# Performance work log

Measured on AMD Instinct MI355X. Metric: run time of the kernel, lower is better.

## Reference

```python
import jax, jax.numpy as jnp
import numpy as np

N = 49104   # anchors (from hardcoded [2, 49104, 80] in source)
C = 80      # classes
K = 100     # max detections kept per class (fixed for jit-able output shapes)
SCORE_THRESH = 0.05
IOU_THRESH = 0.5


def setup_inputs() -> dict:
    key = jax.random.key(0)
    k1, k2 = jax.random.split(key)
    scores = jax.random.uniform(k1, (N, C), dtype=jnp.float32)
    # build valid xyxy boxes inside an ~800x800 image
    r = jax.random.uniform(k2, (N, 4), dtype=jnp.float32)
    x1 = r[:, 0] * 768.0
    y1 = r[:, 1] * 768.0
    w = r[:, 2] * 96.0 + 4.0
    h = r[:, 3] * 96.0 + 4.0
    boxes = jnp.stack([x1, y1, x1 + w, y1 + h], axis=1)
    return {"scores": scores, "boxes": boxes}


def _nms_all(scores, boxes):
    """Per-class greedy NMS, vectorized over classes via vmap.
    scores: [N, C], boxes: [N, 4] xyxy. Returns idxs/scs/valid each [C, K]."""
    areas = (boxes[:, 2] - boxes[:, 0]) * (boxes[:, 3] - boxes[:, 1])  # [N]

    def iou_vs_all(b, b_area):  # b: [4]
        ix1 = jnp.maximum(b[0], boxes[:, 0])
        iy1 = jnp.maximum(b[1], boxes[:, 1])
        ix2 = jnp.minimum(b[2], boxes[:, 2])
        iy2 = jnp.minimum(b[3], boxes[:, 3])
        inter = jnp.clip(ix2 - ix1, 0.0) * jnp.clip(iy2 - iy1, 0.0)
        return inter / (b_area + areas - inter + 1e-8)  # [N]

    def nms_one_class(s_c):  # s_c: [N]
        # score threshold (matches `scores > 0.05` masking in the torch loop)
        s0 = jnp.where(s_c > SCORE_THRESH, s_c, -jnp.inf)

        def step(s, _):
            idx = jnp.argmax(s)
            sc = s[idx]
            keep = jnp.isfinite(sc)  # anything left above threshold?
            ious = iou_vs_all(boxes[idx], areas[idx])
            suppress = (ious > IOU_THRESH) & keep
            s_next = jnp.where(suppress, -jnp.inf, s).at[idx].set(-jnp.inf)
            return s_next, (idx, sc, keep)

        _, (idxs, scs, keeps) = jax.lax.scan(step, s0, None, length=K)
        return idxs, scs, keeps  # each [K]

    return jax.vmap(nms_one_class)(scores.T)  # map over C classes


def reference(scores, boxes):
    idxs, scs, valids = _nms_all(scores, boxes)  # [C, K] each
    idxs = idxs.reshape(-1)                       # [C*K]
    valids = valids.reshape(-1)                   # [C*K] bool
    final_scores = jnp.where(valids, scs.reshape(-1), 0.0)        # [C*K]
    final_classes = jnp.repeat(jnp.arange(C, dtype=jnp.int32), K)  # [C*K]
    final_boxes = boxes[idxs] * valids[:, None].astype(boxes.dtype)  # [C*K, 4]
    return final_scores, final_classes, final_boxes, valids
```

## Files before the change

kernel.cpp:

```cpp
#include <hip/hip_runtime.h>
#include <math.h>
#include <stdint.h>

#define N_ANCH 49104
#define NCLS 80
#define KDET 100
#define CAP 256
#define TPB 512
#define NBINS 1024
#define NPROD 384
#define NBLK NPROD
#define NCONS NCLS
#define GRID (NPROD + NCONS)
#define SUBCAP 16
#define THETA 0.996090f
#define QTOT (N_ANCH * NCLS / 4)
#define JMAX 16
#define FLAG_MAGIC 0x5AC10000u
#define PADKEY(t) ((0xFFFFFFFFull << 16) | (uint64_t)(t))

#define LIST_ELEMS ((size_t)NCLS * NBLK * SUBCAP)
#define SUBCNT_OFF (LIST_ELEMS * 8)
#define FLAGS_OFF (SUBCNT_OFF + (size_t)NCLS * NBLK * 4)
#define WS_NEED (FLAGS_OFF + (size_t)NPROD * 4)

__device__ __forceinline__ void st_agent_u64(uint64_t* p, uint64_t v) {
    __hip_atomic_store(p, v, __ATOMIC_RELAXED, __HIP_MEMORY_SCOPE_AGENT);
}
__device__ __forceinline__ void st_agent_u32(int* p, int v) {
    __hip_atomic_store(p, v, __ATOMIC_RELAXED, __HIP_MEMORY_SCOPE_AGENT);
}
__device__ __forceinline__ uint64_t ld_agent_u64(const uint64_t* p) {
    return __hip_atomic_load(p, __ATOMIC_RELAXED, __HIP_MEMORY_SCOPE_AGENT);
}
__device__ __forceinline__ int ld_agent_i32(const int* p) {
    return __hip_atomic_load(p, __ATOMIC_RELAXED, __HIP_MEMORY_SCOPE_AGENT);
}
__device__ __forceinline__ uint32_t ld_agent_flag(const uint32_t* p) {
    return __hip_atomic_load(p, __ATOMIC_RELAXED, __HIP_MEMORY_SCOPE_AGENT);
}

__device__ __forceinline__ void collect_quad(int q, float4 v, int* lcnt,
                                             uint64_t* __restrict__ list, int blk) {
    const int n = q / 20;
    const int c0 = 4 * (q % 20);
    float ss[4] = {v.x, v.y, v.z, v.w};
#pragma unroll
    for (int u = 0; u < 4; u++) {
        float s = ss[u];
        if (s > THETA) {
            int c = c0 + u;
            int p = atomicAdd(&lcnt[c], 1);
            if (p < SUBCAP) {
                uint32_t bits = __float_as_uint(s);
                st_agent_u64(&list[((size_t)c * NBLK + blk) * SUBCAP + p],
                             ((uint64_t)(~bits) << 16) | (uint64_t)n);
            }
        }
    }
}

struct ChunkShared {
    uint64_t keys[CAP];
    float4   rbox[CAP];
    float    ra[CAP], rs[CAP];
    uint64_t smat[CAP * (CAP / 64)];
    uint64_t lwbuf[CAP / 64];
    uint64_t s_kw[CAP / 64];
    int      s_cw[4];
    float4   kbox[KDET];
    float    kar[KDET], ksc[KDET];
};

__device__ __forceinline__ int process_chunk(ChunkShared& S, int tid, int M, int kc0,
                                             const float* __restrict__ boxes) {
    if (M <= 0) return kc0;
    const int lane = tid & 63, wid = tid >> 6;
    if (tid < CAP) {
        const uint64_t key = S.keys[tid];
        const int n = (int)(key & 0xFFFFull);
        const int nc = n < N_ANCH ? n : N_ANCH - 1;
        const float4 mybox = *(const float4*)(boxes + (size_t)nc * 4);
        int rank = 0;
#pragma unroll 8
        for (int j = 0; j < CAP; j++) rank += (S.keys[j] < key) ? 1 : 0;
        S.rbox[rank] = mybox;
        S.ra[rank] = (mybox.z - mybox.x) * (mybox.w - mybox.y);
        S.rs[rank] = __uint_as_float(~((uint32_t)(key >> 16)));
    }
    __syncthreads();
    bool alive = (tid < M);
    if (alive && kc0 > 0) {
        float4 b = S.rbox[tid];
        float arb = S.ra[tid];
        for (int k2 = 0; k2 < kc0; k2++) {
            float4 kb = S.kbox[k2];
            float ix1 = fmaxf(kb.x, b.x), iy1 = fmaxf(kb.y, b.y);
            float ix2 = fminf(kb.z, b.z), iy2 = fminf(kb.w, b.w);
            float inter = fmaxf(ix2 - ix1, 0.0f) * fmaxf(iy2 - iy1, 0.0f);
            float iou = inter / (S.kar[k2] + arb - inter + 1e-8f);
            if (iou > 0.5f) { alive = false; break; }
        }
    }
    {
        uint64_t bal = __ballot(alive);
        if (lane == 0 && wid < 4) S.lwbuf[wid] = bal;
    }
    __syncthreads();
    for (int p = wid; p < 10; p += 8) {
        const int vw = (int)((0x3333222110ull >> (4 * p)) & 0xF);
        const int ws = (int)((0x3210210100ull >> (4 * p)) & 0xF);
        const int i0 = vw << 6;
        if (i0 >= M) continue;
        const int i1 = min(M, i0 + 64);
        const int jj = (ws << 6) + lane;
        float4 bj = S.rbox[jj];
        float arj = S.ra[jj];
        float4 bi = S.rbox[i0];
        float ari = S.ra[i0];
        for (int i = i0; i < i1; i++) {
            float4 bin = bi; float arin = ari;
            if (i + 1 < i1) { bin = S.rbox[i + 1]; arin = S.ra[i + 1]; }
            bool bit = false;
            if (jj < i) {
                float ix1 = fmaxf(bj.x, bi.x), iy1 = fmaxf(bj.y, bi.y);
                float ix2 = fminf(bj.z, bi.z), iy2 = fminf(bj.w, bi.w);
                float inter = fmaxf(ix2 - ix1, 0.0f) * fmaxf(iy2 - iy1, 0.0f);
                float iou = inter / (arj + ari - inter + 1e-8f);
                bit = iou > 0.5f;
            }
            uint64_t bb = __ballot(bit);
            if (lane == 0) S.smat[((size_t)i << 2) + ws] = bb;
            bi = bin; ari = arin;
        }
    }
    __syncthreads();
    uint64_t st0 = 0, st1 = 0, st2 = 0, st3 = 0;
    if (tid < M) {
        st0 = S.smat[((size_t)tid << 2) + 0];
        if (wid >= 1) st1 = S.smat[((size_t)tid << 2) + 1];
        if (wid >= 2) st2 = S.smat[((size_t)tid << 2) + 2];
        if (wid >= 3) st3 = S.smat[((size_t)tid << 2) + 3];
    }
    bool kept = alive;
    bool converged = false;
    for (int it = 0; it < JMAX; it++) {
        uint64_t kb = __ballot(kept);
        if (lane == 0 && wid < 4) S.s_kw[wid] = kb;
        __syncthreads();
        const uint64_t k0 = S.s_kw[0], k1 = S.s_kw[1], k2 = S.s_kw[2], k3 = S.s_kw[3];
        const bool sup = ((k0 & st0) | (k1 & st1) | (k2 & st2) | (k3 & st3)) != 0ull;
        const bool nk = alive && !sup;
        uint64_t cb = __ballot(nk != kept);
        if (lane == 0 && wid < 4) S.s_cw[wid] = (cb != 0ull) ? 1 : 0;
        kept = nk;
        __syncthreads();
        if ((S.s_cw[0] | S.s_cw[1] | S.s_cw[2] | S.s_cw[3]) == 0) { converged = true; break; }
    }
    if (!converged) {
        if (tid == 0) {
            uint64_t lv[4] = {S.lwbuf[0], S.lwbuf[1], S.lwbuf[2], S.lwbuf[3]};
            uint64_t kw[4] = {0, 0, 0, 0};
            for (int i = 0; i < M; i++) {
                const int w = i >> 6, b = i & 63;
                if (!((lv[w] >> b) & 1ull)) continue;
                const uint64_t* row = &S.smat[(size_t)i << 2];
                uint64_t sup = kw[0] & row[0];
                if (w >= 1) sup |= kw[1] & row[1];
                if (w >= 2) sup |= kw[2] & row[2];
                if (w >= 3) sup |= kw[3] & row[3];
                if (!sup) kw[w] |= 1ull << b;
            }
            S.s_kw[0] = kw[0]; S.s_kw[1] = kw[1]; S.s_kw[2] = kw[2]; S.s_kw[3] = kw[3];
        }
        __syncthreads();
    }
    const uint64_t k0 = S.s_kw[0], k1 = S.s_kw[1], k2 = S.s_kw[2], k3 = S.s_kw[3];
    const int total = __popcll(k0) + __popcll(k1) + __popcll(k2) + __popcll(k3);
    const uint64_t mykw = (wid == 0) ? k0 : (wid == 1) ? k1 : (wid == 2) ? k2 : k3;
    if (tid < M && ((mykw >> lane) & 1ull)) {
        int rk = __popcll(mykw & ((1ull << lane) - 1ull));
        if (wid > 0) rk += __popcll(k0);
        if (wid > 1) rk += __popcll(k1);
        if (wid > 2) rk += __popcll(k2);
        const int r = kc0 + rk;
        if (r < KDET) { S.kbox[r] = S.rbox[tid]; S.kar[r] = S.ra[tid]; S.ksc[r] = S.rs[tid]; }
    }
    __syncthreads();
    return min(kc0 + total, KDET);
}

__device__ __forceinline__ int slow_path(ChunkShared& S, int* hist, int* s_cnt, int* s_lo,
                                         int c, int kc, bool fast, int tid,
                                         const float* __restrict__ scores,
                                         const float* __restrict__ boxes) {
    const float hicut = fast ? THETA : 3.0e38f;
    if (!fast) kc = 0;
    for (int b = tid; b < NBINS; b += TPB) hist[b] = 0;
    __syncthreads();
    for (int n = tid; n < N_ANCH; n += TPB) {
        float s = scores[(size_t)n * NCLS + c];
        if (s > 0.05f && s <= hicut) {
            int b = (int)(s * 1024.0f);
            b = b < 0 ? 0 : (b > NBINS - 1 ? NBINS - 1 : b);
            atomicAdd(&hist[b], 1);
        }
    }
    __syncthreads();
    int hi = NBINS;
    while (hi > 0 && kc < KDET) {
        if (tid == 0) {
            int lo = hi, tot = 0;
            while (lo > 0 && tot + hist[lo - 1] <= CAP) { lo--; tot += hist[lo]; }
            if (lo == hi) lo = hi - 1;
            *s_lo = lo; *s_cnt = 0;
        }
        if (tid < CAP) S.keys[tid] = PADKEY(tid);
        __syncthreads();
        const int lo = *s_lo;
        for (int n = tid; n < N_ANCH; n += TPB) {
            float s = scores[(size_t)n * NCLS + c];
            if (s > 0.05f && s <= hicut) {
                int b = (int)(s * 1024.0f);
                b = b < 0 ? 0 : (b > NBINS - 1 ? NBINS - 1 : b);
                if (b >= lo && b < hi) {
                    int p = atomicAdd(s_cnt, 1);
                    if (p < CAP) {
                        uint32_t bits = __float_as_uint(s);
                        S.keys[p] = ((uint64_t)(~bits) << 16) | (uint64_t)n;
                    }
                }
            }
        }
        __syncthreads();
        const int M2 = min(*s_cnt, CAP);
        kc = process_chunk(S, tid, M2, kc, boxes);
        hi = lo;
    }
    return kc;
}

__device__ __forceinline__ void write_outputs(ChunkShared& S, int c, int kc, int tid,
                                              float* __restrict__ out) {
    float* o_sc = out;
    float* o_cl = out + NCLS * KDET;
    float* o_bx = out + 2 * NCLS * KDET;
    float* o_va = out + 6 * NCLS * KDET;
    for (int k = tid; k < KDET; k += TPB) {
        bool valid = k < kc;
        o_sc[c * KDET + k] = valid ? S.ksc[k] : 0.0f;
        o_cl[c * KDET + k] = (float)c;
        o_va[c * KDET + k] = valid ? 1.0f : 0.0f;
        float4 bo;
        if (valid) bo = S.kbox[k];
        else { bo.x = 0.0f; bo.y = 0.0f; bo.z = 0.0f; bo.w = 0.0f; }
        *(float4*)(o_bx + ((size_t)(c * KDET + k)) * 4) = bo;
    }
}

__global__ __launch_bounds__(TPB) void nms_pc(const float* __restrict__ scores,
                                              const float* __restrict__ boxes,
                                              uint64_t* __restrict__ list,
                                              int* __restrict__ subcnt,
                                              uint32_t* __restrict__ flags,
                                              float* __restrict__ out) {
    const int blk = blockIdx.x, tid = threadIdx.x;
    const int lane = tid & 63, wid = tid >> 6;
    __shared__ ChunkShared S;
    __shared__ int hist[NBINS];
    __shared__ int lcnt[NCLS];
    __shared__ int s_wtot[TPB / 64];
    __shared__ int s_ov, s_cnt, s_lo;

    if (blk < NPROD) {
        for (int cc = tid; cc < NCLS; cc += TPB) lcnt[cc] = 0;
        __syncthreads();
        const float4* sc4 = (const float4*)scores;
        const int stride = NPROD * TPB;
        int q = blk * TPB + tid;
        for (; q + 3 * stride < QTOT; q += 4 * stride) {
            float4 v0 = sc4[q], v1 = sc4[q + stride];
            float4 v2 = sc4[q + 2 * stride], v3 = sc4[q + 3 * stride];
            collect_quad(q, v0, lcnt, list, blk);
            collect_quad(q + stride, v1, lcnt, list, blk);
            collect_quad(q + 2 * stride, v2, lcnt, list, blk);
            collect_quad(q + 3 * stride, v3, lcnt, list, blk);
        }
        for (; q < QTOT; q += stride) collect_quad(q, sc4[q], lcnt, list, blk);
        __syncthreads();
        for (int cc = tid; cc < NCLS; cc += TPB) st_agent_u32(&subcnt[cc * NBLK + blk], lcnt[cc]);
        __syncthreads();
        if (tid == 0)
            __hip_atomic_store(&flags[blk], FLAG_MAGIC | (uint32_t)blk,
                               __ATOMIC_RELEASE, __HIP_MEMORY_SCOPE_AGENT);
        return;
    }

    const int c = blk - NPROD;
    if (tid < CAP) S.keys[tid] = PADKEY(tid);
    if (tid == 0) s_ov = 0;
    {
        bool ready = (tid >= NBLK);
        const uint32_t exp0 = FLAG_MAGIC | (uint32_t)tid;
        while (true) {
            if (!ready) ready = (ld_agent_flag(&flags[tid]) == exp0);
            if (__syncthreads_and((int)ready)) break;
            __builtin_amdgcn_s_sleep(2);
        }
    }
    int kc = 0;
    bool fast = false;
    {
        int raw = 0;
        if (tid < NBLK) raw = ld_agent_i32(&subcnt[c * NBLK + tid]);
        if (raw > SUBCAP) atomicOr(&s_ov, 1);
        const int v = (tid < NBLK) ? min(raw, SUBCAP) : 0;
        int incl = v;
        for (int d = 1; d < 64; d <<= 1) {
            int o = __shfl_up(incl, d, 64);
            if (lane >= d) incl += o;
        }
        if (lane == 63) s_wtot[wid] = incl;
        __syncthreads();
        int woff = 0;
        for (int w = 0; w < wid; w++) woff += s_wtot[w];
        const int off = woff + incl - v;
        int M0 = 0;
        for (int w = 0; w < TPB / 64; w++) M0 += s_wtot[w];
        fast = (s_ov == 0) && (M0 <= CAP);
        if (fast && v > 0) {
            const uint64_t* src = list + ((size_t)c * NBLK + tid) * SUBCAP;
            for (int k = 0; k < v; k++) S.keys[off + k] = ld_agent_u64(&src[k]);
        }
        __syncthreads();
        if (fast) kc = process_chunk(S, tid, M0, 0, boxes);
    }
    if (kc < KDET) kc = slow_path(S, hist, &s_cnt, &s_lo, c, kc, fast, tid, scores, boxes);
    __syncthreads();
    write_outputs(S, c, kc, tid, out);
}

__global__ __launch_bounds__(TPB) void nms_slow(const float* __restrict__ scores,
                                                const float* __restrict__ boxes,
                                                float* __restrict__ out) {
    const int c = blockIdx.x, tid = threadIdx.x;
    __shared__ ChunkShared S;
    __shared__ int hist[NBINS];
    __shared__ int s_cnt, s_lo;
    int kc = slow_path(S, hist, &s_cnt, &s_lo, c, 0, false, tid, scores, boxes);
    __syncthreads();
    write_outputs(S, c, kc, tid, out);
}

extern "C" void kernel_launch(void* const* d_in, const int* in_sizes, int n_in,
                              void* d_out, int out_size, void* d_ws, size_t ws_size,
                              hipStream_t stream) {
    const float* scores = (const float*)d_in[0];
    const float* boxes  = (const float*)d_in[1];
    float* out = (float*)d_out;

    if (ws_size >= WS_NEED) {
        uint64_t* list   = (uint64_t*)d_ws;
        int*      subcnt = (int*)((char*)d_ws + SUBCNT_OFF);
        uint32_t* flags  = (uint32_t*)((char*)d_ws + FLAGS_OFF);
        nms_pc<<<GRID, TPB, 0, stream>>>(scores, boxes, list, subcnt, flags, out);
        return;
    }
    nms_slow<<<NCLS, TPB, 0, stream>>>(scores, boxes, out);
}
```

Measured before the change: 94.83 us.

## Merge producer and consumer blocks, double block size, trim chunk rank work

Replaces the separate 384 producer blocks and 80 consumer blocks with 144 blocks of 1024 threads. Every block first collects candidates, and the first 80 then go on to run per-class NMS. The rank computation now scans only M keys with 128-bit loads, and the suppression-matrix build spreads its tiles over 16 waves instead of 8. Key padding per chunk is dropped. The aim is fewer blocks, less idle waiting and more threads on the per-class sequential part, at the cost of lower occupancy and reliance on all 144 blocks being co-resident for the spin-wait. Dropping the padding means the rank loop and the rest of the chunk logic must not read stale keys past M.

```diff
diff --git a/kernel.cpp b/kernel.cpp
--- a/kernel.cpp
+++ b/kernel.cpp
@@ -6,12 +6,11 @@
 #define NCLS 80
 #define KDET 100
 #define CAP 256
-#define TPB 512
+#define TPB 1024
 #define NBINS 1024
-#define NPROD 384
-#define NBLK NPROD
-#define NCONS NCLS
-#define GRID (NPROD + NCONS)
+#define NBLK 144
+#define NCONS 80
+#define GRID NBLK
 #define SUBCAP 16
 #define THETA 0.996090f
 #define QTOT (N_ANCH * NCLS / 4)
@@ -22,7 +21,7 @@
 #define LIST_ELEMS ((size_t)NCLS * NBLK * SUBCAP)
 #define SUBCNT_OFF (LIST_ELEMS * 8)
 #define FLAGS_OFF (SUBCNT_OFF + (size_t)NCLS * NBLK * 4)
-#define WS_NEED (FLAGS_OFF + (size_t)NPROD * 4)
+#define WS_NEED (FLAGS_OFF + (size_t)NBLK * 4)
 
 __device__ __forceinline__ void st_agent_u64(uint64_t* p, uint64_t v) {
     __hip_atomic_store(p, v, __ATOMIC_RELAXED, __HIP_MEMORY_SCOPE_AGENT);
@@ -76,14 +75,19 @@
                                              const float* __restrict__ boxes) {
     if (M <= 0) return kc0;
     const int lane = tid & 63, wid = tid >> 6;
-    if (tid < CAP) {
+    if (tid < M) {
         const uint64_t key = S.keys[tid];
         const int n = (int)(key & 0xFFFFull);
-        const int nc = n < N_ANCH ? n : N_ANCH - 1;
-        const float4 mybox = *(const float4*)(boxes + (size_t)nc * 4);
+        const float4 mybox = *(const float4*)(boxes + (size_t)n * 4);
         int rank = 0;
-#pragma unroll 8
-        for (int j = 0; j < CAP; j++) rank += (S.keys[j] < key) ? 1 : 0;
+        const int Me = M & ~1;
+#pragma unroll 4
+        for (int j = 0; j < Me; j += 2) {
+            const ulonglong2 kk = *(const ulonglong2*)&S.keys[j];
+            rank += (kk.x < key) ? 1 : 0;
+            rank += (kk.y < key) ? 1 : 0;
+        }
+        if (Me < M) rank += (S.keys[Me] < key) ? 1 : 0;
         S.rbox[rank] = mybox;
         S.ra[rank] = (mybox.z - mybox.x) * (mybox.w - mybox.y);
         S.rs[rank] = __uint_as_float(~((uint32_t)(key >> 16)));
@@ -107,31 +111,32 @@
         if (lane == 0 && wid < 4) S.lwbuf[wid] = bal;
     }
     __syncthreads();
-    for (int p = wid; p < 10; p += 8) {
+    {
+        int p, istart, istep;
+        if (wid < 12) { p = wid >> 1; istart = wid & 1; istep = 2; }
+        else          { p = wid - 6;  istart = 0;       istep = 1; }
         const int vw = (int)((0x3333222110ull >> (4 * p)) & 0xF);
         const int ws = (int)((0x3210210100ull >> (4 * p)) & 0xF);
         const int i0 = vw << 6;
-        if (i0 >= M) continue;
-        const int i1 = min(M, i0 + 64);
-        const int jj = (ws << 6) + lane;
-        float4 bj = S.rbox[jj];
-        float arj = S.ra[jj];
-        float4 bi = S.rbox[i0];
-        float ari = S.ra[i0];
-        for (int i = i0; i < i1; i++) {
-            float4 bin = bi; float arin = ari;
-            if (i + 1 < i1) { bin = S.rbox[i + 1]; arin = S.ra[i + 1]; }
-            bool bit = false;
-            if (jj < i) {
-                float ix1 = fmaxf(bj.x, bi.x), iy1 = fmaxf(bj.y, bi.y);
-                float ix2 = fminf(bj.z, bi.z), iy2 = fminf(bj.w, bi.w);
-                float inter = fmaxf(ix2 - ix1, 0.0f) * fmaxf(iy2 - iy1, 0.0f);
-                float iou = inter / (arj + ari - inter + 1e-8f);
-                bit = iou > 0.5f;
+        if (i0 < M) {
+            const int i1 = min(M, i0 + 64);
+            const int jj = (ws << 6) + lane;
+            float4 bj = S.rbox[jj];
+            float arj = S.ra[jj];
+            for (int i = i0 + istart; i < i1; i += istep) {
+                bool bit = false;
+                if (jj < i) {
+                    float4 bi = S.rbox[i];
+                    float ari = S.ra[i];
+                    float ix1 = fmaxf(bj.x, bi.x), iy1 = fmaxf(bj.y, bi.y);
+                    float ix2 = fminf(bj.z, bi.z), iy2 = fminf(bj.w, bi.w);
+                    float inter = fmaxf(ix2 - ix1, 0.0f) * fmaxf(iy2 - iy1, 0.0f);
+                    float iou = inter / (arj + ari - inter + 1e-8f);
+                    bit = iou > 0.5f;
+                }
+                uint64_t bb = __ballot(bit);
+                if (lane == 0) S.smat[((size_t)i << 2) + ws] = bb;
             }
-            uint64_t bb = __ballot(bit);
-            if (lane == 0) S.smat[((size_t)i << 2) + ws] = bb;
-            bi = bin; ari = arin;
         }
     }
     __syncthreads();
@@ -215,7 +220,6 @@
             if (lo == hi) lo = hi - 1;
             *s_lo = lo; *s_cnt = 0;
         }
-        if (tid < CAP) S.keys[tid] = PADKEY(tid);
         __syncthreads();
         const int lo = *s_lo;
         for (int n = tid; n < N_ANCH; n += TPB) {
@@ -272,11 +276,11 @@
     __shared__ int s_wtot[TPB / 64];
     __shared__ int s_ov, s_cnt, s_lo;
 
-    if (blk < NPROD) {
-        for (int cc = tid; cc < NCLS; cc += TPB) lcnt[cc] = 0;
-        __syncthreads();
+    for (int cc = tid; cc < NCLS; cc += TPB) lcnt[cc] = 0;
+    __syncthreads();
+    {
         const float4* sc4 = (const float4*)scores;
-        const int stride = NPROD * TPB;
+        const int stride = GRID * TPB;
         int q = blk * TPB + tid;
         for (; q + 3 * stride < QTOT; q += 4 * stride) {
             float4 v0 = sc4[q], v1 = sc4[q + stride];
@@ -287,17 +291,16 @@
             collect_quad(q + 3 * stride, v3, lcnt, list, blk);
         }
         for (; q < QTOT; q += stride) collect_quad(q, sc4[q], lcnt, list, blk);
-        __syncthreads();
-        for (int cc = tid; cc < NCLS; cc += TPB) st_agent_u32(&subcnt[cc * NBLK + blk], lcnt[cc]);
-        __syncthreads();
-        if (tid == 0)
-            __hip_atomic_store(&flags[blk], FLAG_MAGIC | (uint32_t)blk,
-                               __ATOMIC_RELEASE, __HIP_MEMORY_SCOPE_AGENT);
-        return;
-    }
-
-    const int c = blk - NPROD;
-    if (tid < CAP) S.keys[tid] = PADKEY(tid);
+    }
+    __syncthreads();
+    for (int cc = tid; cc < NCLS; cc += TPB) st_agent_u32(&subcnt[cc * NBLK + blk], lcnt[cc]);
+    __syncthreads();
+    if (tid == 0)
+        __hip_atomic_store(&flags[blk], FLAG_MAGIC | (uint32_t)blk,
+                           __ATOMIC_RELEASE, __HIP_MEMORY_SCOPE_AGENT);
+    if (blk >= NCONS) return;
+
+    const int c = blk;
     if (tid == 0) s_ov = 0;
     {
         bool ready = (tid >= NBLK);
```

Result: faster. 83.98 us (-11.4%).
